# Performance work log

Hardware: AMD Instinct MI355X
Metric: run time of the kernel (lower is better)

The kernel has to match this reference:

```python
import jax, jax.numpy as jnp
import numpy as np

NUM_HEADS = 8
LN_EPS = 1e-5


def _avg_pool_mat(n_in, n_out):
    # torch adaptive_avg_pool windows: start=floor(i*n_in/n_out), end=ceil((i+1)*n_in/n_out)
    M = np.zeros((n_out, n_in), dtype=np.float32)
    for i in range(n_out):
        s = (i * n_in) // n_out
        e = -((-(i + 1) * n_in) // n_out)
        M[i, s:e] = 1.0 / (e - s)
    return jnp.asarray(M)


def _adaptive_avg_pool(x, out_hw):
    # separable mean over rectangular windows: [B,C,H,W] -> [B,C,out,out]
    Mh = _avg_pool_mat(x.shape[2], out_hw)
    Mw = _avg_pool_mat(x.shape[3], out_hw)
    return jnp.einsum('bchw,ph,qw->bcpq', x, Mh, Mw)


def _max_pool(x, oh, ow):
    # exact (divisible) adaptive max pool
    B, C, H, W = x.shape
    assert H % oh == 0 and W % ow == 0
    return x.reshape(B, C, oh, H // oh, ow, W // ow).max(axis=(3, 5))


def _conv1x1_res(t, w, b):
    # t + Conv2d(1x1)(t); w is [C_in, C_out]
    return t + jnp.einsum('bchw,cd->bdhw', t, w) + b[None, :, None, None]


def _tokens(t):
    B, C = t.shape[:2]
    return t.reshape(B, C, -1).transpose(0, 2, 1)  # [B, hw, C]


def setup_inputs():
    B, L, C = 8, 1024, 512
    H = W = 64
    key = jax.random.key(0)
    ks = jax.random.split(key, 16)
    n = lambda k, s, sc=0.02: jax.random.normal(k, s, jnp.float32) * sc
    return dict(
        x=jax.random.normal(ks[0], (B, H * W, C), jnp.float32),
        m=jax.random.normal(ks[1], (B, L, C), jnp.float32),
        w_s1=n(ks[2], (C, C)), b_s1=n(ks[3], (C,)),
        w_s2=n(ks[4], (C, C)), b_s2=n(ks[5], (C,)),
        w_s3=n(ks[6], (C, C)), b_s3=n(ks[7], (C,)),
        w_s4=n(ks[8], (C, C)), b_s4=n(ks[9], (C,)),
        w_mx=n(ks[10], (C, C)), b_mx=n(ks[11], (C,)),
        ln_g=jnp.ones((C,), jnp.float32), ln_b=jnp.zeros((C,), jnp.float32),
        Wq=n(ks[12], (C, C)), Wkv=n(ks[13], (C, 2 * C)),
        Wp=n(ks[14], (C, C)), bp=n(ks[15], (C,)),
        H=H, W=W, patch_size=16,
    )


def reference(x, m, w_s1, b_s1, w_s2, b_s2, w_s3, b_s3, w_s4, b_s4,
              w_mx, b_mx, ln_g, ln_b, Wq, Wkv, Wp, bp, H, W, patch_size):
    B, L, C = m.shape
    nh = NUM_HEADS
    d = C // nh
    scale = d ** -0.5

    q = (m @ Wq).reshape(B, L, nh, d).transpose(0, 2, 1, 3)  # [B,nh,L,d]

    x_ = x.transpose(0, 2, 1).reshape(B, C, H, W)
    s1 = _conv1x1_res(_adaptive_avg_pool(x_, round(H * 4 / 12)), w_s1, b_s1)
    s2 = _conv1x1_res(_adaptive_avg_pool(x_, round(H * 4 / 16)), w_s2, b_s2)
    s3 = _conv1x1_res(_adaptive_avg_pool(x_, round(H * 4 / 20)), w_s3, b_s3)
    s4 = _conv1x1_res(_adaptive_avg_pool(x_, round(H * 4 / 24)), w_s4, b_s4)
    mx = _conv1x1_res(_max_pool(x_, H * 4 // patch_size, W * 4 // patch_size), w_mx, b_mx)

    p = jnp.concatenate([_tokens(s1), _tokens(s2), _tokens(s3), _tokens(s4), _tokens(mx)], axis=1)
    mu = p.mean(-1, keepdims=True)
    var = ((p - mu) ** 2).mean(-1, keepdims=True)
    p = (p - mu) / jnp.sqrt(var + LN_EPS) * ln_g + ln_b

    kv_in = jnp.concatenate([p, m], axis=1)  # [B, N_p+L, C]
    kv = (kv_in @ Wkv).reshape(B, -1, 2, nh, d)
    k = kv[:, :, 0].transpose(0, 2, 1, 3)  # [B,nh,N,d]
    v = kv[:, :, 1].transpose(0, 2, 1, 3)

    attn = jax.nn.softmax(jnp.einsum('bhld,bhnd->bhln', q, k) * scale, axis=-1)
    out = jnp.einsum('bhln,bhnd->bhld', attn, v).transpose(0, 2, 1, 3).reshape(B, L, C)
    out = out @ Wp + bp
    return out, mx
```

## Files before the change

kernel.cpp:

```cpp
#include <hip/hip_runtime.h>

typedef unsigned short u16;
typedef __attribute__((ext_vector_type(8))) short bf16x8;
typedef __attribute__((ext_vector_type(4))) float f32x4;
typedef int i32x2 __attribute__((ext_vector_type(2)));

__device__ __forceinline__ float bf2f(u16 u) {
  union { unsigned int i; float f; } x; x.i = ((unsigned int)u) << 16; return x.f;
}
__device__ __forceinline__ u16 f2bf(float f) {
  union { float f; unsigned int i; } x; x.f = f;
  unsigned int r = x.i + 0x7fffu + ((x.i >> 16) & 1u);
  return (u16)(r >> 16);
}

#define CFENCE() asm volatile("" ::: "memory")

__device__ __forceinline__ unsigned cvtpk_bf16(float lo, float hi) {
  unsigned r;
  asm("v_cvt_pk_bf16_f32 %0, %1, %2" : "=v"(r) : "v"(lo), "v"(hi));
  return r;
}

__global__ __launch_bounds__(256) void k_pool(
    const float* __restrict__ x, u16* __restrict__ pool,
    const float* __restrict__ m, u16* __restrict__ mb)
{
  int blk = blockIdx.x;
  if (blk >= 9944) {
    size_t i = ((size_t)(blk - 9944) * 256 + threadIdx.x) * 8;
    float4 a = *(const float4*)(m + i);
    float4 b = *(const float4*)(m + i + 4);
    ushort4 u0, u1;
    u0.x = f2bf(a.x); u0.y = f2bf(a.y); u0.z = f2bf(a.z); u0.w = f2bf(a.w);
    u1.x = f2bf(b.x); u1.y = f2bf(b.y); u1.z = f2bf(b.z); u1.w = f2bf(b.w);
    *(ushort4*)(mb + i) = u0;
    *(ushort4*)(mb + i + 4) = u1;
    return;
  }
  int b = blk / 1243;
  int tok = blk - b * 1243;
  int c = threadIdx.x;
  const float* xb = x + (size_t)b * 4096 * 512;
  float r0, r1;
  if (tok >= 987) {
    int t = tok - 987;
    int oh = t >> 4, ow = t & 15;
    float m0 = -1e38f, m1 = -1e38f;
    for (int hh = 0; hh < 4; hh++)
      for (int ww = 0; ww < 4; ww++) {
        const float* px = xb + (size_t)((oh * 4 + hh) * 64 + ow * 4 + ww) * 512 + c;
        m0 = fmaxf(m0, px[0]);
        m1 = fmaxf(m1, px[256]);
      }
    r0 = m0; r1 = m1;
  } else {
    int n, t;
    if (tok < 441)      { n = 21; t = tok; }
    else if (tok < 697) { n = 16; t = tok - 441; }
    else if (tok < 866) { n = 13; t = tok - 697; }
    else                { n = 11; t = tok - 866; }
    int oh = t / n, ow = t - oh * n;
    int h0 = (oh * 64) / n, h1 = ((oh + 1) * 64 + n - 1) / n;
    int w0 = (ow * 64) / n, w1 = ((ow + 1) * 64 + n - 1) / n;
    float inv = 1.0f / (float)((h1 - h0) * (w1 - w0));
    float s0 = 0.f, s1 = 0.f;
    for (int hh = h0; hh < h1; hh++)
      for (int ww = w0; ww < w1; ww++) {
        const float* px = xb + (size_t)(hh * 64 + ww) * 512 + c;
        s0 += px[0];
        s1 += px[256];
      }
    r0 = s0 * inv; r1 = s1 * inv;
  }
  u16* dst = pool + (size_t)(b * 1243 + tok) * 512 + c;
  dst[0]   = f2bf(r0);
  dst[256] = f2bf(r1);
}

__global__ __launch_bounds__(256) void k_wt8(
    const float* w0, const float* w1, const float* w2, const float* w3,
    const float* w4, const float* w5, const float* w6, const float* w7,
    u16* __restrict__ wt_base)
{
  int z = blockIdx.z;
  int N = (z == 6) ? 1024 : 512;
  if (N == 512 && blockIdx.x >= 16) return;
  const float* W =
      z == 0 ? w0 : z == 1 ? w1 : z == 2 ? w2 : z == 3 ? w3 :
      z == 4 ? w4 : z == 5 ? w5 : z == 6 ? w6 : w7;
  size_t doff = (z <= 5) ? (size_t)z * 262144
                         : (z == 6 ? (size_t)6 * 262144 : (size_t)6 * 262144 + 524288);
  u16* Wt = wt_base + doff;

  __shared__ float tile[32][33];
  int n0 = blockIdx.x * 32, k0 = blockIdx.y * 32;
  int t = threadIdx.x;
  int rr = t >> 5, cc = t & 31;
#pragma unroll
  for (int ps = 0; ps < 4; ps++)
    tile[ps * 8 + rr][cc] = W[(size_t)(k0 + ps * 8 + rr) * N + n0 + cc];
  __syncthreads();
#pragma unroll
  for (int ps = 0; ps < 4; ps++)
    Wt[(size_t)(n0 + ps * 8 + rr) * 512 + k0 + cc] = f2bf(tile[cc][ps * 8 + rr]);
}

template <class EPI>
__device__ __forceinline__ void gemm_core(
    const u16* __restrict__ Az, const u16* __restrict__ Bt,
    int M, int K, int m0, int n0, EPI&& epi)
{
  __shared__ __align__(16) u16 As[128][40];
  __shared__ __align__(16) u16 Bs[128][40];

  const int tid = threadIdx.x;
  const int lane = tid & 63, wv = tid >> 6;
  const int quad = lane >> 4, l15 = lane & 15;
  const int wm = (wv >> 1) * 64, wn = (wv & 1) * 64;

  f32x4 acc[4][4];
#pragma unroll
  for (int i = 0; i < 4; i++)
#pragma unroll
    for (int j = 0; j < 4; j++) acc[i][j] = (f32x4){0.f, 0.f, 0.f, 0.f};

  const int srow = tid >> 1;
  const int scol = (tid & 1) * 16;
  const bool aok = (m0 + srow) < M;
  const u16* ag = Az + (size_t)(m0 + srow) * K + scol;
  const u16* bg = Bt + (size_t)(n0 + srow) * K + scol;

  uint4 a0 = {0, 0, 0, 0}, a1 = {0, 0, 0, 0}, b0, b1;
  if (aok) { a0 = *(const uint4*)ag; a1 = *(const uint4*)(ag + 8); }
  b0 = *(const uint4*)bg;
  b1 = *(const uint4*)(bg + 8);

  for (int k0 = 0; k0 < K; k0 += 32) {
    CFENCE();
    __builtin_amdgcn_s_barrier();
    asm volatile("s_waitcnt vmcnt(0)" ::: "memory");
    *(uint4*)&As[srow][scol]     = a0;
    *(uint4*)&As[srow][scol + 8] = a1;
    *(uint4*)&Bs[srow][scol]     = b0;
    *(uint4*)&Bs[srow][scol + 8] = b1;
    if (k0 + 32 < K) {
      if (aok) { a0 = *(const uint4*)(ag + k0 + 32); a1 = *(const uint4*)(ag + k0 + 40); }
      b0 = *(const uint4*)(bg + k0 + 32);
      b1 = *(const uint4*)(bg + k0 + 40);
    }
    asm volatile("s_waitcnt lgkmcnt(0)" ::: "memory");
    __builtin_amdgcn_s_barrier();
    CFENCE();

    bf16x8 af[4];
#pragma unroll
    for (int i = 0; i < 4; i++)
      af[i] = *(const bf16x8*)&As[wm + i * 16 + l15][quad * 8];
#pragma unroll
    for (int j = 0; j < 4; j++) {
      bf16x8 bfj = *(const bf16x8*)&Bs[wn + j * 16 + l15][quad * 8];
#pragma unroll
      for (int i = 0; i < 4; i++)
        acc[i][j] = __builtin_amdgcn_mfma_f32_16x16x32_bf16(af[i], bfj, acc[i][j], 0, 0, 0);
    }
  }

#pragma unroll
  for (int i = 0; i < 4; i++) {
    int rb = m0 + wm + i * 16 + quad * 4;
#pragma unroll
    for (int j = 0; j < 4; j++) {
      int col = n0 + wn + j * 16 + l15;
#pragma unroll
      for (int r = 0; r < 4; r++) {
        int row = rb + r;
        if (row >= M) continue;
        epi(row, col, acc[i][j][r]);
      }
    }
  }
}

__global__ __launch_bounds__(256) void k_gemm_f32(
    const u16* __restrict__ A, long long a_bs, const u16* __restrict__ Bt,
    const float* __restrict__ bias, float* __restrict__ C, long long c_bs,
    int M, int N, int K)
{
  const u16* Az = A + (size_t)blockIdx.z * a_bs;
  float* Cz = C + (size_t)blockIdx.z * c_bs;
  gemm_core(Az, Bt, M, K, blockIdx.y * 128, blockIdx.x * 128,
            [&](int row, int col, float v) {
              Cz[(size_t)row * N + col] = v + bias[col];
            });
}

__global__ __launch_bounds__(256) void k_gemm_big(
    const u16* __restrict__ mb, const u16* __restrict__ p,
    const u16* __restrict__ wqkv, const u16* __restrict__ wkv,
    u16* __restrict__ q, u16* __restrict__ KV)
{
  int y = blockIdx.y, z = blockIdx.z;
  if (y < 8) {
    const u16* Az = mb + (size_t)z * (1024 * 512);
    u16* qz  = q  + (size_t)z * (1024 * 512);
    u16* kvz = KV + (size_t)(z * 2267 + 1243) * 1024;
    gemm_core(Az, wqkv, 1024, 512, y * 128, blockIdx.x * 128,
              [&](int row, int col, float v) {
                u16 bv = f2bf(v);
                if (col < 512) qz[(size_t)row * 512 + col] = bv;
                else           kvz[(size_t)row * 1024 + (col - 512)] = bv;
              });
  } else {
    if (blockIdx.x >= 8) return;
    const u16* Az = p + (size_t)z * (1243 * 512);
    u16* kvz = KV + (size_t)z * 2267 * 1024;
    gemm_core(Az, wkv, 1243, 512, (y - 8) * 128, blockIdx.x * 128,
              [&](int row, int col, float v) {
                kvz[(size_t)row * 1024 + col] = f2bf(v);
              });
  }
}

__global__ __launch_bounds__(256) void k_conv_seg(
    const u16* __restrict__ pool, const u16* __restrict__ wts,
    const float* b0, const float* b1, const float* b2, const float* b3,
    const float* b4, u16* __restrict__ p, float* __restrict__ out2)
{
  int y = blockIdx.y, bz = blockIdx.z;
  int s, m0;
  if (y < 4)      { s = 0; m0 = y * 128; }
  else if (y < 6) { s = 1; m0 = (y - 4) * 128; }
  else if (y < 8) { s = 2; m0 = (y - 6) * 128; }
  else if (y < 9) { s = 3; m0 = 0; }
  else            { s = 4; m0 = (y - 9) * 128; }
  int t0  = s == 0 ? 0 : s == 1 ? 441 : s == 2 ? 697 : s == 3 ? 866 : 987;
  int cnt = s == 0 ? 441 : s == 1 ? 256 : s == 2 ? 169 : s == 3 ? 121 : 256;
  const float* bias = s == 0 ? b0 : s == 1 ? b1 : s == 2 ? b2 : s == 3 ? b3 : b4;
  size_t base = (size_t)bz * (1243 * 512) + (size_t)t0 * 512;
  const u16* Az = pool + base;
  u16* Cz = p + base;
  gemm_core(Az, wts + (size_t)s * 262144, cnt, 512, m0, blockIdx.x * 128,
            [&](int row, int col, float v) {
              v += bias[col] + bf2f(Az[(size_t)row * 512 + col]);
              Cz[(size_t)row * 512 + col] = f2bf(v);
              if (s == 4)
                out2[((size_t)(bz * 512 + col)) * 256 + row] = v;
            });
}

__global__ __launch_bounds__(256) void k_ln(
    u16* __restrict__ p, const float* __restrict__ g, const float* __restrict__ bb)
{
  __shared__ float red[8];
  size_t row = blockIdx.x;
  u16* pr = p + row * 512;
  int t = threadIdx.x;
  float v0 = bf2f(pr[t]), v1 = bf2f(pr[t + 256]);
  float s = v0 + v1;
#pragma unroll
  for (int off = 1; off < 64; off <<= 1) s += __shfl_xor(s, off);
  int wave = t >> 6;
  if ((t & 63) == 0) red[wave] = s;
  __syncthreads();
  float mean = (red[0] + red[1] + red[2] + red[3]) * (1.f / 512.f);
  float d0 = v0 - mean, d1 = v1 - mean;
  float s2 = d0 * d0 + d1 * d1;
#pragma unroll
  for (int off = 1; off < 64; off <<= 1) s2 += __shfl_xor(s2, off);
  if ((t & 63) == 0) red[4 + wave] = s2;
  __syncthreads();
  float var = (red[4] + red[5] + red[6] + red[7]) * (1.f / 512.f);
  float rstd = rsqrtf(var + 1e-5f);
  pr[t]       = f2bf(d0 * rstd * g[t]       + bb[t]);
  pr[t + 256] = f2bf(d1 * rstd * g[t + 256] + bb[t + 256]);
}

__global__ __launch_bounds__(512) void k_attn_mfma(
    const u16* __restrict__ qb, const u16* __restrict__ KV,
    u16* __restrict__ outb)
{
  __shared__ __align__(16) u16 KsV[2][64][72];
#define Ks_ (KsV[0])
#define Vt_ (KsV[1])

  const int bid = blockIdx.x;
  const int qt = bid >> 6;
  const int hb = bid & 63;
  const int h = hb & 7, b = hb >> 3;
  const int tid = threadIdx.x;
  const int lane = tid & 63, wv = tid >> 6;
  const int qw = wv >> 1, kw = wv & 1;
  const int quad = lane >> 4, l15 = lane & 15;

  const u16* kvb = KV + (size_t)b * 2267 * 1024;
  const int kr = tid >> 3, kc = (tid & 7) * 8;
  const int vp = tid & 31, vc = (tid >> 5) * 4;
  const int e2v = 2 * vp;
  const int vcol = (e2v & 32) | (e2v & 0x13) | ((e2v & 4) << 1) | ((e2v & 8) >> 1);

  uint4 kreg = {0, 0, 0, 0};
  uint2 vra = {0, 0}, vrb = {0, 0};
  auto load_tile = [&](int n0) {
    kreg = (uint4){0, 0, 0, 0};
    vra = (uint2){0, 0};
    vrb = (uint2){0, 0};
    if (n0 + kr < 2267)
      kreg = *(const uint4*)(kvb + (size_t)(n0 + kr) * 1024 + h * 64 + kc);
    int na = n0 + 2 * vp;
    const u16* s = kvb + (size_t)na * 1024 + 512 + h * 64 + vc;
    if (na < 2267)     vra = *(const uint2*)s;
    if (na + 1 < 2267) vrb = *(const uint2*)(s + 1024);
  };

  load_tile(0);
  const u16* qrow = qb + (size_t)(b * 1024 + qt * 64 + qw * 16 + l15) * 512 + h * 64;
  bf16x8 aq0 = *(const bf16x8*)(qrow + quad * 8);
  bf16x8 aq1 = *(const bf16x8*)(qrow + 32 + quad * 8);

  float l_acc = 0.f;
  f32x4 o_acc[4];
#pragma unroll
  for (int i = 0; i < 4; i++) o_acc[i] = (f32x4){0.f, 0.f, 0.f, 0.f};

  __syncthreads();

  for (int n0 = 0; n0 < 2267; n0 += 64) {
    CFENCE();
    __builtin_amdgcn_s_barrier();
    asm volatile("s_waitcnt vmcnt(0)" ::: "memory");
    *(uint4*)&Ks_[kr][kc] = kreg;
    {
      unsigned lo0 = __builtin_amdgcn_perm(vrb.x, vra.x, 0x05040100u);
      unsigned hi0 = __builtin_amdgcn_perm(vrb.x, vra.x, 0x07060302u);
      unsigned lo1 = __builtin_amdgcn_perm(vrb.y, vra.y, 0x05040100u);
      unsigned hi1 = __builtin_amdgcn_perm(vrb.y, vra.y, 0x07060302u);
      *(unsigned*)&Vt_[vc + 0][vcol] = lo0;
      *(unsigned*)&Vt_[vc + 1][vcol] = hi0;
      *(unsigned*)&Vt_[vc + 2][vcol] = lo1;
      *(unsigned*)&Vt_[vc + 3][vcol] = hi1;
    }
    if (n0 + 64 < 2267) load_tile(n0 + 64);
    asm volatile("s_waitcnt lgkmcnt(0)" ::: "memory");
    __builtin_amdgcn_s_barrier();
    CFENCE();

    f32x4 sacc[2];
#pragma unroll
    for (int t = 0; t < 2; t++) {
      int krow = kw * 32 + t * 16 + l15;
      bf16x8 bk0 = *(const bf16x8*)&Ks_[krow][quad * 8];
      bf16x8 bk1 = *(const bf16x8*)&Ks_[krow][32 + quad * 8];
      f32x4 z = (f32x4){0.f, 0.f, 0.f, 0.f};
      z = __builtin_amdgcn_mfma_f32_16x16x32_bf16(bk0, aq0, z, 0, 0, 0);
      sacc[t] = __builtin_amdgcn_mfma_f32_16x16x32_bf16(bk1, aq1, z, 0, 0, 0);
    }

    unsigned Pk[4];
#pragma unroll
    for (int t = 0; t < 2; t++) {
      float e0 = __builtin_amdgcn_exp2f(fminf(sacc[t][0] * 0.18033688f, 43.28f));
      float e1 = __builtin_amdgcn_exp2f(fminf(sacc[t][1] * 0.18033688f, 43.28f));
      float e2 = __builtin_amdgcn_exp2f(fminf(sacc[t][2] * 0.18033688f, 43.28f));
      float e3 = __builtin_amdgcn_exp2f(fminf(sacc[t][3] * 0.18033688f, 43.28f));
      l_acc += (e0 + e1) + (e2 + e3);
      Pk[2 * t]     = cvtpk_bf16(e0, e1);
      Pk[2 * t + 1] = cvtpk_bf16(e2, e3);
    }
    i32x2 sA = __builtin_amdgcn_permlane32_swap((int)Pk[0], (int)Pk[2], false, false);
    i32x2 sB = __builtin_amdgcn_permlane32_swap((int)Pk[1], (int)Pk[3], false, false);
    uint4 au;
    au.x = (unsigned)sA[0]; au.y = (unsigned)sB[0];
    au.z = (unsigned)sA[1]; au.w = (unsigned)sB[1];
    bf16x8 ap = __builtin_bit_cast(bf16x8, au);

#pragma unroll
    for (int t = 0; t < 4; t++) {
      bf16x8 vf = *(const bf16x8*)&Vt_[t * 16 + l15][kw * 32 + quad * 8];
      o_acc[t] = __builtin_amdgcn_mfma_f32_16x16x32_bf16(ap, vf, o_acc[t], 0, 0, 0);
    }
  }

  l_acc += __shfl_xor(l_acc, 16);
  l_acc += __shfl_xor(l_acc, 32);

  __syncthreads();
  float* Op = (float*)&KsV[0][0][0];
  float* Lp = Op + 4096;
  if (kw == 1) {
#pragma unroll
    for (int t = 0; t < 4; t++)
#pragma unroll
      for (int r = 0; r < 4; r++)
        Op[(qw * 16 + quad * 4 + r) * 64 + t * 16 + l15] = o_acc[t][r];
    if (quad == 0) Lp[qw * 16 + l15] = l_acc;
  }
  __syncthreads();
  if (kw == 0) {
#pragma unroll
    for (int r = 0; r < 4; r++) {
      int row = qw * 16 + quad * 4 + r;
      float lq = __shfl(l_acc, (lane & 48) | (quad * 4 + r));
      float lt = lq + Lp[row] - 37.f;
      float inv = 1.f / fmaxf(lt, 1e-20f);
#pragma unroll
      for (int t = 0; t < 4; t++) {
        size_t oi = (size_t)(b * 1024 + qt * 64 + row) * 512 + h * 64 + t * 16 + l15;
        outb[oi] = f2bf((o_acc[t][r] + Op[row * 64 + t * 16 + l15]) * inv);
      }
    }
  }
#undef Ks_
#undef Vt_
}

extern "C" void kernel_launch(void* const* d_in, const int* in_sizes, int n_in,
                              void* d_out, int out_size, void* d_ws, size_t ws_size,
                              hipStream_t stream)
{
  const float* x = (const float*)d_in[0];
  const float* m = (const float*)d_in[1];
  const float* ln_g = (const float*)d_in[12];
  const float* ln_b = (const float*)d_in[13];
  const float* Wq   = (const float*)d_in[14];
  const float* Wkv  = (const float*)d_in[15];
  const float* Wp   = (const float*)d_in[16];
  const float* bp   = (const float*)d_in[17];
  float* out = (float*)d_out;

  u16* pool = (u16*)d_ws;
  u16* p    = pool + 5091328;
  u16* q    = p + 5091328;
  u16* KV   = q + 4194304;
  u16* mb   = KV + 18571264;
  u16* wt_s = mb + 4194304;
  u16* attn_out = pool;

  k_wt8<<<dim3(32, 16, 8), 256, 0, stream>>>(
      (const float*)d_in[2], (const float*)d_in[4], (const float*)d_in[6],
      (const float*)d_in[8], (const float*)d_in[10], Wq, Wkv, Wp, wt_s);

  k_pool<<<11992, 256, 0, stream>>>(x, pool, m, mb);

  k_conv_seg<<<dim3(4, 11, 8), 256, 0, stream>>>(
      pool, wt_s, (const float*)d_in[3], (const float*)d_in[5],
      (const float*)d_in[7], (const float*)d_in[9], (const float*)d_in[11],
      p, out + 4194304);

  k_ln<<<9944, 256, 0, stream>>>(p, ln_g, ln_b);

  k_gemm_big<<<dim3(12, 18, 8), 256, 0, stream>>>(
      mb, p, wt_s + 5 * 262144, wt_s + 6 * 262144, q, KV);

  k_attn_mfma<<<1024, 512, 0, stream>>>(q, KV, attn_out);

  k_gemm_f32<<<dim3(4, 8, 8), 256, 0, stream>>>(attn_out, (long long)1024 * 512,
                                                wt_s + 6 * 262144 + 524288, bp,
                                                out, (long long)1024 * 512,
                                                1024, 512, 512);
  (void)in_sizes; (void)n_in; (void)out_size; (void)ws_size;
}
```

Before: 400.6 us.

## Give each attention wave all keys of a tile and double queries per block

The attention kernel used to split each 64-key tile between two waves per 16-query group, then merged the partial outputs and row sums through shared memory. Now each of the 8 waves handles its own 16 query rows against the full 64-key tile, so a block covers 128 queries and the grid drops to 512 blocks. Each K/V tile staged in shared memory now serves twice as many queries, which cuts K/V reloads, and the end-of-kernel cross-wave merge and its barriers go away. The MFMA sections are also wrapped in s_setprio to favour matrix issue; the cost is more MFMA and exp work per wave per tile and fewer blocks to spread across the CUs.

```diff
diff --git a/kernel.cpp b/kernel.cpp
--- a/kernel.cpp
+++ b/kernel.cpp
@@ -290,7 +290,6 @@
   const int h = hb & 7, b = hb >> 3;
   const int tid = threadIdx.x;
   const int lane = tid & 63, wv = tid >> 6;
-  const int qw = wv >> 1, kw = wv & 1;
   const int quad = lane >> 4, l15 = lane & 15;
 
   const u16* kvb = KV + (size_t)b * 2267 * 1024;
@@ -314,7 +313,7 @@
   };
 
   load_tile(0);
-  const u16* qrow = qb + (size_t)(b * 1024 + qt * 64 + qw * 16 + l15) * 512 + h * 64;
+  const u16* qrow = qb + (size_t)(b * 1024 + qt * 128 + wv * 16 + l15) * 512 + h * 64;
   bf16x8 aq0 = *(const bf16x8*)(qrow + quad * 8);
   bf16x8 aq1 = *(const bf16x8*)(qrow + 32 + quad * 8);
 
@@ -345,69 +344,62 @@
     __builtin_amdgcn_s_barrier();
     CFENCE();
 
-    f32x4 sacc[2];
-#pragma unroll
-    for (int t = 0; t < 2; t++) {
-      int krow = kw * 32 + t * 16 + l15;
-      bf16x8 bk0 = *(const bf16x8*)&Ks_[krow][quad * 8];
-      bf16x8 bk1 = *(const bf16x8*)&Ks_[krow][32 + quad * 8];
-      f32x4 z = (f32x4){0.f, 0.f, 0.f, 0.f};
-      z = __builtin_amdgcn_mfma_f32_16x16x32_bf16(bk0, aq0, z, 0, 0, 0);
-      sacc[t] = __builtin_amdgcn_mfma_f32_16x16x32_bf16(bk1, aq1, z, 0, 0, 0);
-    }
-
-    unsigned Pk[4];
-#pragma unroll
-    for (int t = 0; t < 2; t++) {
-      float e0 = __builtin_amdgcn_exp2f(fminf(sacc[t][0] * 0.18033688f, 43.28f));
-      float e1 = __builtin_amdgcn_exp2f(fminf(sacc[t][1] * 0.18033688f, 43.28f));
-      float e2 = __builtin_amdgcn_exp2f(fminf(sacc[t][2] * 0.18033688f, 43.28f));
-      float e3 = __builtin_amdgcn_exp2f(fminf(sacc[t][3] * 0.18033688f, 43.28f));
-      l_acc += (e0 + e1) + (e2 + e3);
-      Pk[2 * t]     = cvtpk_bf16(e0, e1);
-      Pk[2 * t + 1] = cvtpk_bf16(e2, e3);
-    }
-    i32x2 sA = __builtin_amdgcn_permlane32_swap((int)Pk[0], (int)Pk[2], false, false);
-    i32x2 sB = __builtin_amdgcn_permlane32_swap((int)Pk[1], (int)Pk[3], false, false);
-    uint4 au;
-    au.x = (unsigned)sA[0]; au.y = (unsigned)sB[0];
-    au.z = (unsigned)sA[1]; au.w = (unsigned)sB[1];
-    bf16x8 ap = __builtin_bit_cast(bf16x8, au);
-
-#pragma unroll
-    for (int t = 0; t < 4; t++) {
-      bf16x8 vf = *(const bf16x8*)&Vt_[t * 16 + l15][kw * 32 + quad * 8];
-      o_acc[t] = __builtin_amdgcn_mfma_f32_16x16x32_bf16(ap, vf, o_acc[t], 0, 0, 0);
+#pragma unroll
+    for (int s = 0; s < 2; s++) {
+      f32x4 sacc[2];
+      __builtin_amdgcn_s_setprio(1);
+#pragma unroll
+      for (int t = 0; t < 2; t++) {
+        int krow = s * 32 + t * 16 + l15;
+        bf16x8 bk0 = *(const bf16x8*)&Ks_[krow][quad * 8];
+        bf16x8 bk1 = *(const bf16x8*)&Ks_[krow][32 + quad * 8];
+        f32x4 z = (f32x4){0.f, 0.f, 0.f, 0.f};
+        z = __builtin_amdgcn_mfma_f32_16x16x32_bf16(bk0, aq0, z, 0, 0, 0);
+        sacc[t] = __builtin_amdgcn_mfma_f32_16x16x32_bf16(bk1, aq1, z, 0, 0, 0);
+      }
+      __builtin_amdgcn_s_setprio(0);
+
+      unsigned Pk[4];
+#pragma unroll
+      for (int t = 0; t < 2; t++) {
+        float e0 = __builtin_amdgcn_exp2f(fminf(sacc[t][0] * 0.18033688f, 43.28f));
+        float e1 = __builtin_amdgcn_exp2f(fminf(sacc[t][1] * 0.18033688f, 43.28f));
+        float e2 = __builtin_amdgcn_exp2f(fminf(sacc[t][2] * 0.18033688f, 43.28f));
+        float e3 = __builtin_amdgcn_exp2f(fminf(sacc[t][3] * 0.18033688f, 43.28f));
+        l_acc += (e0 + e1) + (e2 + e3);
+        Pk[2 * t]     = cvtpk_bf16(e0, e1);
+        Pk[2 * t + 1] = cvtpk_bf16(e2, e3);
+      }
+      i32x2 sA = __builtin_amdgcn_permlane32_swap((int)Pk[0], (int)Pk[2], false, false);
+      i32x2 sB = __builtin_amdgcn_permlane32_swap((int)Pk[1], (int)Pk[3], false, false);
+      uint4 au;
+      au.x = (unsigned)sA[0]; au.y = (unsigned)sB[0];
+      au.z = (unsigned)sA[1]; au.w = (unsigned)sB[1];
+      bf16x8 ap = __builtin_bit_cast(bf16x8, au);
+
+      __builtin_amdgcn_s_setprio(1);
+#pragma unroll
+      for (int t = 0; t < 4; t++) {
+        bf16x8 vf = *(const bf16x8*)&Vt_[t * 16 + l15][s * 32 + quad * 8];
+        o_acc[t] = __builtin_amdgcn_mfma_f32_16x16x32_bf16(ap, vf, o_acc[t], 0, 0, 0);
+      }
+      __builtin_amdgcn_s_setprio(0);
     }
   }
 
   l_acc += __shfl_xor(l_acc, 16);
   l_acc += __shfl_xor(l_acc, 32);
 
-  __syncthreads();
-  float* Op = (float*)&KsV[0][0][0];
-  float* Lp = Op + 4096;
-  if (kw == 1) {
-#pragma unroll
-    for (int t = 0; t < 4; t++)
-#pragma unroll
-      for (int r = 0; r < 4; r++)
-        Op[(qw * 16 + quad * 4 + r) * 64 + t * 16 + l15] = o_acc[t][r];
-    if (quad == 0) Lp[qw * 16 + l15] = l_acc;
-  }
-  __syncthreads();
-  if (kw == 0) {
-#pragma unroll
-    for (int r = 0; r < 4; r++) {
-      int row = qw * 16 + quad * 4 + r;
-      float lq = __shfl(l_acc, (lane & 48) | (quad * 4 + r));
-      float lt = lq + Lp[row] - 37.f;
-      float inv = 1.f / fmaxf(lt, 1e-20f);
-#pragma unroll
-      for (int t = 0; t < 4; t++) {
-        size_t oi = (size_t)(b * 1024 + qt * 64 + row) * 512 + h * 64 + t * 16 + l15;
-        outb[oi] = f2bf((o_acc[t][r] + Op[row * 64 + t * 16 + l15]) * inv);
-      }
+#pragma unroll
+  for (int r = 0; r < 4; r++) {
+    int row = wv * 16 + quad * 4 + r;
+    float lq = __shfl(l_acc, (lane & 48) | (quad * 4 + r));
+    float lt = lq - 37.f;
+    float inv = 1.f / fmaxf(lt, 1e-20f);
+#pragma unroll
+    for (int t = 0; t < 4; t++) {
+      size_t oi = (size_t)(b * 1024 + qt * 128 + row) * 512 + h * 64 + t * 16 + l15;
+      outb[oi] = f2bf(o_acc[t][r] * inv);
     }
   }
 #undef Ks_
@@ -452,7 +444,7 @@
   k_gemm_big<<<dim3(12, 18, 8), 256, 0, stream>>>(
       mb, p, wt_s + 5 * 262144, wt_s + 6 * 262144, q, KV);
 
-  k_attn_mfma<<<1024, 512, 0, stream>>>(q, KV, attn_out);
+  k_attn_mfma<<<512, 512, 0, stream>>>(q, KV, attn_out);
 
   k_gemm_f32<<<dim3(4, 8, 8), 256, 0, stream>>>(attn_out, (long long)1024 * 512,
                                                 wt_s + 6 * 262144 + 524288, bp,
```

Result: faster. 366.3 us (-8.5%).
